# Performance work log

Hardware: AMD Instinct MI355X
Metric: run time of the kernel (lower is better)

Reference implementation:

```python
import jax, jax.numpy as jnp
import numpy as np

B, T, F, H = 512, 365, 16, 256


def _lstm_layer(x, W_ih, W_hh, b_ih, b_hh):
    """batch_first LSTM layer, torch gate order (i, f, g, o).
    x: [B, T, in]. Returns (outputs [B, T, H], final h [B, H])."""
    # Precompute input projections for all timesteps: [T, B, 4H]
    x_proj = jnp.einsum('bti,gi->tbg', x, W_ih) + (b_ih + b_hh)
    h0 = jnp.zeros((x.shape[0], W_hh.shape[1]), x.dtype)
    c0 = jnp.zeros_like(h0)

    def step(carry, xp):
        h, c = carry
        z = xp + h @ W_hh.T  # [B, 4H]
        i, f, g, o = jnp.split(z, 4, axis=-1)
        c = jax.nn.sigmoid(f) * c + jax.nn.sigmoid(i) * jnp.tanh(g)
        h = jax.nn.sigmoid(o) * jnp.tanh(c)
        return (h, c), h

    (hT, _), hs = jax.lax.scan(step, (h0, c0), x_proj)
    return jnp.transpose(hs, (1, 0, 2)), hT


def setup_inputs() -> dict:
    key = jax.random.key(0)
    ks = jax.random.split(key, 11)
    s1 = 1.0 / np.sqrt(H)
    u = lambda k, shape: jax.random.uniform(k, shape, jnp.float32, -s1, s1)
    return {
        'x': jax.random.normal(ks[0], (B, T, F), jnp.float32),
        'W_ih1': u(ks[1], (4 * H, F)),
        'W_hh1': u(ks[2], (4 * H, H)),
        'b_ih1': u(ks[3], (4 * H,)),
        'b_hh1': u(ks[4], (4 * H,)),
        'W_ih2': u(ks[5], (4 * H, H)),
        'W_hh2': u(ks[6], (4 * H, H)),
        'b_ih2': u(ks[7], (4 * H,)),
        'b_hh2': u(ks[8], (4 * H,)),
        'W_lin': u(ks[9], (1, H)),
        'b_lin': u(ks[10], (1,)),
    }


def reference(x, W_ih1, W_hh1, b_ih1, b_hh1, W_ih2, W_hh2, b_ih2, b_hh2, W_lin, b_lin):
    h1_seq, _ = _lstm_layer(x, W_ih1, W_hh1, b_ih1, b_hh1)
    # dropout(p=0.1) is identity in eval mode
    _, hT = _lstm_layer(h1_seq, W_ih2, W_hh2, b_ih2, b_hh2)
    out = (hT @ W_lin.T + b_lin).reshape(-1)  # [B]
    return out
```

## Files before the change

### kernel.cpp

```cpp
#include <hip/hip_runtime.h>


#define T_STEPS 365
#define RS 564

typedef __attribute__((ext_vector_type(8))) short short8;
typedef __attribute__((ext_vector_type(4))) float float4_;
typedef __attribute__((ext_vector_type(4))) unsigned int uint4_;
typedef unsigned long long u64;
typedef unsigned int u32;

#define MFMA16(a, b, c) __builtin_amdgcn_mfma_f32_16x16x32_bf16((a), (b), (c), 0, 0, 0)

__device__ __forceinline__ unsigned short f2bf(float v) {
    union { float f; u32 u; } a; a.f = v;
    u32 r = a.u + 0x7fffu + ((a.u >> 16) & 1u);
    return (unsigned short)(r >> 16);
}
__device__ __forceinline__ float bf2f(unsigned short h) {
    union { u32 u; float f; } a; a.u = ((u32)h) << 16; return a.f;
}
__device__ __forceinline__ u32 packhl(float v) {
    unsigned short hi = f2bf(v);
    unsigned short lo = f2bf(v - bf2f(hi));
    return ((u32)hi << 16) | (u32)lo;
}
__device__ __forceinline__ float sigm(float x)  { return 1.f / (1.f + __expf(-x)); }
__device__ __forceinline__ float tanh_(float x) { return 2.f / (1.f + __expf(-2.f * x)) - 1.f; }

__device__ __forceinline__ void unpk(uint4_ a, uint4_ b, short8& hi, short8& lo) {
    union U { u32 d[4]; short8 s; } H, L;
    H.d[0] = __builtin_amdgcn_perm(a.y, a.x, 0x07060302u);
    H.d[1] = __builtin_amdgcn_perm(a.w, a.z, 0x07060302u);
    H.d[2] = __builtin_amdgcn_perm(b.y, b.x, 0x07060302u);
    H.d[3] = __builtin_amdgcn_perm(b.w, b.z, 0x07060302u);
    L.d[0] = __builtin_amdgcn_perm(a.y, a.x, 0x05040100u);
    L.d[1] = __builtin_amdgcn_perm(a.w, a.z, 0x05040100u);
    L.d[2] = __builtin_amdgcn_perm(b.y, b.x, 0x05040100u);
    L.d[3] = __builtin_amdgcn_perm(b.w, b.z, 0x05040100u);
    hi = H.s; lo = L.s;
}

__global__ void prep_w(
    const float* __restrict__ Wih1, const float* __restrict__ Whh1,
    const float* __restrict__ bih1, const float* __restrict__ bhh1,
    const float* __restrict__ Wih2, const float* __restrict__ Whh2,
    const float* __restrict__ bih2, const float* __restrict__ bhh2,
    unsigned short* __restrict__ w1h, unsigned short* __restrict__ w1l,
    unsigned short* __restrict__ w2h, unsigned short* __restrict__ w2l,
    float* __restrict__ bias1, float* __restrict__ bias2)
{
    const int tile = blockIdx.x;
    const int g = tile >> 4, ns = tile & 15;
    const int tid = threadIdx.x;

    for (int idx = tid; idx < 9 * 512; idx += 256) {
        int ks = idx >> 9, off = idx & 511, r = off >> 5, kk = off & 31;
        int R = g * 256 + ns * 16 + r;
        float v;
        if (ks < 8)       v = Whh1[R * 256 + ks * 32 + kk];
        else if (kk < 16) v = Wih1[R * 16 + kk];
        else              v = 0.f;
        unsigned short h = f2bf(v);
        size_t d = (size_t)(tile * 9 + ks) * 512 + off;
        w1h[d] = h; w1l[d] = f2bf(v - bf2f(h));
    }
    for (int idx = tid; idx < 16 * 512; idx += 256) {
        int ks = idx >> 9, off = idx & 511, r = off >> 5, kk = off & 31;
        int R = g * 256 + ns * 16 + r;
        int k = ks * 32 + kk;
        float v = (k < 256) ? Wih2[R * 256 + k] : Whh2[R * 256 + (k - 256)];
        unsigned short h = f2bf(v);
        size_t d = (size_t)(tile * 16 + ks) * 512 + off;
        w2h[d] = h; w2l[d] = f2bf(v - bf2f(h));
    }
    if (tid < 16) {
        int R = g * 256 + ns * 16 + tid;
        bias1[R] = bih1[R] + bhh1[R];
        bias2[R] = bih2[R] + bhh2[R];
    }
}

__global__ __launch_bounds__(512, 2) void lstm_main(
    const float* __restrict__ x,
    const unsigned short* __restrict__ w1h, const unsigned short* __restrict__ w1l,
    const unsigned short* __restrict__ w2h, const unsigned short* __restrict__ w2l,
    const float* __restrict__ bias1, const float* __restrict__ bias2,
    u32* hb1, u32* hb2, u32* prog,
    const float* __restrict__ Wlin, const float* __restrict__ blin,
    float* __restrict__ out)
{
    __shared__ __align__(16) u32 A2u[32 * RS];
    __shared__ __align__(16) float zb1[3 * 64 * 36];
    __shared__ __align__(16) float zb2[5 * 64 * 36];
    __shared__ __align__(16) float hp[32][17];

    const int tid  = threadIdx.x;
    const int lane = tid & 63;
    const int wv   = tid >> 6;
    const int quad = lane >> 4;
    const int r16  = lane & 15;
    const int bg   = blockIdx.x & 15;
    const int ns   = blockIdx.x >> 4;

    u32* myprog = prog + bg * 16;

    const bool isL1 = (wv < 3);
    int t0, t1_, t2_, t3_;
    if      (wv == 0) { t0 = 0;  t1_ = 1;  t2_ = 2;  t3_ = -1; }
    else if (wv == 1) { t0 = 3;  t1_ = 4;  t2_ = 5;  t3_ = -1; }
    else if (wv == 2) { t0 = 6;  t1_ = 7;  t2_ = 8;  t3_ = -1; }
    else if (wv == 3) { t0 = 0;  t1_ = 1;  t2_ = 2;  t3_ = 3;  }
    else if (wv == 4) { t0 = 4;  t1_ = 5;  t2_ = 6;  t3_ = -1; }
    else if (wv == 5) { t0 = 7;  t1_ = 9;  t2_ = 10; t3_ = -1; }
    else if (wv == 6) { t0 = 11; t1_ = 12; t2_ = 13; t3_ = -1; }
    else              { t0 = 14; t1_ = 15; t2_ = 16; t3_ = -1; }

    const int loff = r16 * 32 + quad * 8;
    const unsigned short* WHsrc = isL1 ? w1h : w2h;
    const unsigned short* WLsrc = isL1 ? w1l : w2l;
    const int NK = isL1 ? 9 : 16;
    short8 WH[4][4], WL[4][4];
#pragma unroll
    for (int s = 0; s < 4; s++) {
        const int b = (s == 0) ? t0 : (s == 1) ? t1_ : (s == 2) ? t2_ : t3_;
#pragma unroll
        for (int g = 0; g < 4; g++) {
            if (b >= 0) {
                int ks = (!isL1 && b > 8) ? (b - 1) : b;
                size_t off = ((size_t)((g * 16 + ns) * NK + ks)) * 512 + loff;
                WH[g][s] = *(const short8*)(WHsrc + off);
                WL[g][s] = *(const short8*)(WLsrc + off);
            } else {
                WH[g][s] = short8{0,0,0,0,0,0,0,0};
                WL[g][s] = short8{0,0,0,0,0,0,0,0};
            }
        }
    }

    float bi[4] = {0.f, 0.f, 0.f, 0.f};
    if (tid < 256) {
        const float* bsrc = (tid < 128) ? bias1 : bias2;
        int colg = ns * 16 + (tid & 15);
#pragma unroll
        for (int g = 0; g < 4; g++) bi[g] = bsrc[g * 256 + colg];
    }
    float cst[4] = {0.f, 0.f, 0.f, 0.f};

    for (int i = tid; i < 32 * RS; i += 512) A2u[i] = 0u;
    __syncthreads();
    {
        int row = tid >> 4, col = tid & 15;
        float v = x[((size_t)(bg * 32 + row) * T_STEPS + 0) * 16 + col];
        A2u[row * RS + 256 + col] = packhl(v);
    }
    __syncthreads();

    for (int t = 0; t <= T_STEPS; t++) {
        const int p = t & 1;

        float4_ acc[4][2];
        const float4_ z4 = {0.f, 0.f, 0.f, 0.f};
#pragma unroll
        for (int g = 0; g < 4; g++) { acc[g][0] = z4; acc[g][1] = z4; }

#pragma unroll
        for (int s = 0; s < 4; s++) {
            const int b = (s == 0) ? t0 : (s == 1) ? t1_ : (s == 2) ? t2_ : t3_;
            if (b >= 0) {
                const int base0 = r16 * RS + b * 32 + quad * 8;
                uint4_ p00 = *(const uint4_*)&A2u[base0];
                uint4_ p01 = *(const uint4_*)&A2u[base0 + 4];
                uint4_ p10 = *(const uint4_*)&A2u[base0 + 16 * RS];
                uint4_ p11 = *(const uint4_*)&A2u[base0 + 16 * RS + 4];
                short8 ah0, al0, ah1, al1;
                unpk(p00, p01, ah0, al0);
                unpk(p10, p11, ah1, al1);
#pragma unroll
                for (int g = 0; g < 4; g++) {
                    acc[g][0] = MFMA16(ah0, WH[g][s], acc[g][0]);
                    acc[g][0] = MFMA16(al0, WH[g][s], acc[g][0]);
                    acc[g][0] = MFMA16(ah0, WL[g][s], acc[g][0]);
                    acc[g][1] = MFMA16(ah1, WH[g][s], acc[g][1]);
                    acc[g][1] = MFMA16(al1, WH[g][s], acc[g][1]);
                    acc[g][1] = MFMA16(ah1, WL[g][s], acc[g][1]);
                }
            }
        }
        {
            float* zbase = isL1 ? (zb1 + wv * (64 * 36)) : (zb2 + (wv - 3) * (64 * 36));
#pragma unroll
            for (int g = 0; g < 4; g++)
#pragma unroll
                for (int rt = 0; rt < 2; rt++)
                    *(float4_*)&zbase[(size_t)(g * 16 + r16) * 36 + rt * 16 + quad * 4] = acc[g][rt];
        }
        __syncthreads();

        if (tid < 256) {
            const bool is1 = (tid < 128);
            const int hcol = tid & 15;
            const int rq   = (tid >> 4) & 7;
            const float* zb = is1 ? zb1 : zb2;
            const int np = is1 ? 3 : 5;
            float4_ z[4];
#pragma unroll
            for (int g = 0; g < 4; g++) {
                float4_ s = {bi[g], bi[g], bi[g], bi[g]};
#pragma unroll
                for (int pw = 0; pw < 5; pw++) {
                    if (pw < np)
                        s += *(const float4_*)&zb[(size_t)(pw * 64 + g * 16 + hcol) * 36 + rq * 4];
                }
                z[g] = s;
            }
            u32* hb = is1 ? hb1 : hb2;
            const int slot = is1 ? p : (1 - p);
            size_t o = (((size_t)slot * 16 + bg) * 32 + rq * 4) * 256 + ns * 16 + hcol;
#pragma unroll
            for (int j = 0; j < 4; j++) {
                float zi = z[0][j], zf = z[1][j], zg = z[2][j], zo = z[3][j];
                float nc = sigm(zf) * cst[j] + sigm(zi) * tanh_(zg);
                float h  = sigm(zo) * tanh_(nc);
                if (!is1 && t == 0) { nc = 0.f; h = 0.f; }
                cst[j] = nc;
                __hip_atomic_store(&hb[o + (size_t)j * 256], packhl(h),
                                   __ATOMIC_RELAXED, __HIP_MEMORY_SCOPE_AGENT);
            }
        } else {
            const int i0 = tid - 256;
            const int tn = (t + 1 <= T_STEPS - 1) ? (t + 1) : (T_STEPS - 1);
#pragma unroll
            for (int k = 0; k < 2; k++) {
                int idx = i0 + 256 * k;
                int row = idx >> 4, col = idx & 15;
                float v = x[((size_t)(bg * 32 + row) * T_STEPS + tn) * 16 + col];
                A2u[row * RS + 256 + col] = packhl(v);
            }
        }
        __syncthreads();

        if (tid == 0)
            __hip_atomic_store(&myprog[ns], (u32)(t + 1),
                               __ATOMIC_RELAXED, __HIP_MEMORY_SCOPE_AGENT);

        if (t == T_STEPS) break;

        {
            const u32 tgt = (u32)(t + 1);
            while (__hip_atomic_load(&myprog[tid & 15], __ATOMIC_RELAXED,
                                     __HIP_MEMORY_SCOPE_AGENT) < tgt) {}
        }

        {
            const u64* s1 = (const u64*)(hb1 + (size_t)(p * 16 + bg) * 32 * 256);
            const u64* s2 = (const u64*)(hb2 + (size_t)((1 - p) * 16 + bg) * 32 * 256);
#pragma unroll
            for (int j = 0; j < 4; j++) {
                const int row = wv * 4 + j;
                const u64* r1 = s1 + (size_t)row * 128;
                const u64* r2 = s2 + (size_t)row * 128;
                u64 a = __hip_atomic_load(r1 + lane,      __ATOMIC_RELAXED, __HIP_MEMORY_SCOPE_AGENT);
                u64 b = __hip_atomic_load(r1 + 64 + lane, __ATOMIC_RELAXED, __HIP_MEMORY_SCOPE_AGENT);
                u64 c = __hip_atomic_load(r2 + lane,      __ATOMIC_RELAXED, __HIP_MEMORY_SCOPE_AGENT);
                u64 d = __hip_atomic_load(r2 + 64 + lane, __ATOMIC_RELAXED, __HIP_MEMORY_SCOPE_AGENT);
                u32* dst = &A2u[row * RS];
                *(u64*)&dst[2 * lane]             = a;
                *(u64*)&dst[128 + 2 * lane]       = b;
                *(u64*)&dst[288 + 2 * lane]       = c;
                *(u64*)&dst[288 + 128 + 2 * lane] = d;
            }
        }
        __syncthreads();
    }

    if (ns != 0) return;
    {
        const u32 tgt = (u32)(T_STEPS + 1);
        while (__hip_atomic_load(&myprog[tid & 15], __ATOMIC_RELAXED,
                                 __HIP_MEMORY_SCOPE_AGENT) < tgt) {}
    }
    {
        int row = tid >> 4, seg = tid & 15;
        const u32* src = hb2 + ((size_t)bg * 32 + row) * 256 + seg * 16;
        float s = 0.f;
#pragma unroll
        for (int j = 0; j < 16; j++) {
            u32 v = __hip_atomic_load(&src[j], __ATOMIC_RELAXED, __HIP_MEMORY_SCOPE_AGENT);
            s += (bf2f((unsigned short)(v >> 16)) + bf2f((unsigned short)v)) * Wlin[seg * 16 + j];
        }
        hp[row][seg] = s;
    }
    __syncthreads();
    if (tid < 32) {
        float s = 0.f;
#pragma unroll
        for (int j = 0; j < 16; j++) s += hp[tid][j];
        out[bg * 32 + tid] = s + blin[0];
    }
}

extern "C" void kernel_launch(void* const* d_in, const int* in_sizes, int n_in,
                              void* d_out, int out_size, void* d_ws, size_t ws_size,
                              hipStream_t stream) {
    const float* x    = (const float*)d_in[0];
    const float* Wih1 = (const float*)d_in[1];
    const float* Whh1 = (const float*)d_in[2];
    const float* bih1 = (const float*)d_in[3];
    const float* bhh1 = (const float*)d_in[4];
    const float* Wih2 = (const float*)d_in[5];
    const float* Whh2 = (const float*)d_in[6];
    const float* bih2 = (const float*)d_in[7];
    const float* bhh2 = (const float*)d_in[8];
    const float* Wlin = (const float*)d_in[9];
    const float* blin = (const float*)d_in[10];
    float* out = (float*)d_out;

    char* pp = (char*)d_ws;
    unsigned short* w1h = (unsigned short*)pp; pp += (size_t)64 * 9 * 512 * 2;
    unsigned short* w1l = (unsigned short*)pp; pp += (size_t)64 * 9 * 512 * 2;
    unsigned short* w2h = (unsigned short*)pp; pp += (size_t)64 * 16 * 512 * 2;
    unsigned short* w2l = (unsigned short*)pp; pp += (size_t)64 * 16 * 512 * 2;
    float* bias1 = (float*)pp; pp += 1024 * 4;
    float* bias2 = (float*)pp; pp += 1024 * 4;
    char* zero_base = pp;
    u32* hb1 = (u32*)pp; pp += (size_t)2 * 16 * 32 * 256 * 4;
    u32* hb2 = (u32*)pp; pp += (size_t)2 * 16 * 32 * 256 * 4;
    u32* prog = (u32*)pp; pp += 16 * 16 * 4;
    size_t zero_bytes = (size_t)(pp - zero_base);

    hipMemsetAsync(zero_base, 0, zero_bytes, stream);
    prep_w<<<64, 256, 0, stream>>>(Wih1, Whh1, bih1, bhh1, Wih2, Whh2, bih2, bhh2,
                                   w1h, w1l, w2h, w2l, bias1, bias2);
    lstm_main<<<256, 512, 0, stream>>>(x, w1h, w1l, w2h, w2l, bias1, bias2,
                                       hb1, hb2, prog, Wlin, blin, out);
}
```

Before: 2.003 ms.

## Split each batch group into two 16-row chains to overlap exchange with compute

Each block's 32 batch rows become two independent 16-row chains, with separate LDS buffers, progress flags and hidden-state slots. Chain B's GEMM and update run while chain A's cross-block hidden-state exchange is still propagating. Progress is now signalled per wave instead of after a block barrier. A single wave polls the flags with s_sleep and publishes readiness through LDS, so the other waves do not spin on global memory. The cost is more barriers and flag traffic per step, and the hidden-state and flag stores now use workgroup scope, which may weaken cross-block visibility.

```diff
diff --git a/kernel.cpp b/kernel.cpp
--- a/kernel.cpp
+++ b/kernel.cpp
@@ -11,6 +11,7 @@
 typedef unsigned int u32;
 
 #define MFMA16(a, b, c) __builtin_amdgcn_mfma_f32_16x16x32_bf16((a), (b), (c), 0, 0, 0)
+#define LD64(p) __hip_atomic_load((p), __ATOMIC_RELAXED, __HIP_MEMORY_SCOPE_AGENT)
 
 __device__ __forceinline__ unsigned short f2bf(float v) {
     union { float f; u32 u; } a; a.f = v;
@@ -90,10 +91,10 @@
     const float* __restrict__ Wlin, const float* __restrict__ blin,
     float* __restrict__ out)
 {
-    __shared__ __align__(16) u32 A2u[32 * RS];
-    __shared__ __align__(16) float zb1[3 * 64 * 36];
-    __shared__ __align__(16) float zb2[5 * 64 * 36];
+    __shared__ __align__(16) u32 Abuf[2][16 * RS];
+    __shared__ __align__(16) float zbuf[2][8 * 64 * 20];
     __shared__ __align__(16) float hp[32][17];
+    __shared__ u32 rdyv[2];
 
     const int tid  = threadIdx.x;
     const int lane = tid & 63;
@@ -102,8 +103,10 @@
     const int r16  = lane & 15;
     const int bg   = blockIdx.x & 15;
     const int ns   = blockIdx.x >> 4;
-
-    u32* myprog = prog + bg * 16;
+    const int ch0  = bg * 2;
+
+    u32* progA = prog + (size_t)ch0 * 256;
+    u32* progB = prog + (size_t)(ch0 + 1) * 256;
 
     const bool isL1 = (wv < 3);
     int t0, t1_, t2_, t3_;
@@ -138,151 +141,172 @@
         }
     }
 
-    float bi[4] = {0.f, 0.f, 0.f, 0.f};
+    const bool is1u = (tid < 256);
+    const int hcol = tid & 15;
+    const int urow = (tid >> 4) & 15;
+    float bi[4];
+    {
+        const float* bsrc = is1u ? bias1 : bias2;
+        int colg = ns * 16 + hcol;
+#pragma unroll
+        for (int g = 0; g < 4; g++) bi[g] = bsrc[g * 256 + colg];
+    }
+    float cstA = 0.f, cstB = 0.f;
+
+    for (int i = tid; i < 2 * 16 * RS; i += 512) (&Abuf[0][0])[i] = 0u;
+    if (tid < 2) rdyv[tid] = 0u;
+    __syncthreads();
     if (tid < 256) {
-        const float* bsrc = (tid < 128) ? bias1 : bias2;
-        int colg = ns * 16 + (tid & 15);
-#pragma unroll
-        for (int g = 0; g < 4; g++) bi[g] = bsrc[g * 256 + colg];
-    }
-    float cst[4] = {0.f, 0.f, 0.f, 0.f};
-
-    for (int i = tid; i < 32 * RS; i += 512) A2u[i] = 0u;
+        int row = tid >> 4, col = tid & 15;
+        float va = x[((size_t)(bg * 32 + row) * T_STEPS + 0) * 16 + col];
+        float vb = x[((size_t)(bg * 32 + 16 + row) * T_STEPS + 0) * 16 + col];
+        Abuf[0][row * RS + 256 + col] = packhl(va);
+        Abuf[1][row * RS + 256 + col] = packhl(vb);
+    }
     __syncthreads();
-    {
-        int row = tid >> 4, col = tid & 15;
-        float v = x[((size_t)(bg * 32 + row) * T_STEPS + 0) * 16 + col];
-        A2u[row * RS + 256 + col] = packhl(v);
-    }
-    __syncthreads();
+
+#define GEMM_AND_STORE(cidx) do {                                             \
+        float4_ acc[4];                                                       \
+        const float4_ z4 = {0.f, 0.f, 0.f, 0.f};                              \
+        acc[0] = z4; acc[1] = z4; acc[2] = z4; acc[3] = z4;                   \
+        __builtin_amdgcn_s_setprio(1);                                        \
+        _Pragma("unroll")                                                     \
+        for (int s = 0; s < 4; s++) {                                         \
+            const int b = (s == 0) ? t0 : (s == 1) ? t1_ : (s == 2) ? t2_ : t3_; \
+            if (b >= 0) {                                                     \
+                const int base0 = r16 * RS + b * 32 + quad * 8;               \
+                uint4_ p00 = *(const uint4_*)&Abuf[cidx][base0];              \
+                uint4_ p01 = *(const uint4_*)&Abuf[cidx][base0 + 4];          \
+                short8 ah0, al0;                                              \
+                unpk(p00, p01, ah0, al0);                                     \
+                _Pragma("unroll")                                             \
+                for (int g = 0; g < 4; g++) {                                 \
+                    acc[g] = MFMA16(ah0, WH[g][s], acc[g]);                   \
+                    acc[g] = MFMA16(al0, WH[g][s], acc[g]);                   \
+                    acc[g] = MFMA16(ah0, WL[g][s], acc[g]);                   \
+                }                                                             \
+            }                                                                 \
+        }                                                                     \
+        __builtin_amdgcn_s_setprio(0);                                        \
+        _Pragma("unroll")                                                     \
+        for (int g = 0; g < 4; g++)                                           \
+            *(float4_*)&zbuf[cidx][wv * 1280 + (g * 16 + r16) * 20 + quad * 4] = acc[g]; \
+    } while (0)
+
+#define UPDATE_CHAIN(cidx, cstVar, progPtr, ch) do {                          \
+        const float* zb = &zbuf[cidx][(is1u ? 0 : 3) * 1280];                 \
+        const int np = is1u ? 3 : 5;                                          \
+        float z[4];                                                           \
+        _Pragma("unroll")                                                     \
+        for (int g = 0; g < 4; g++) {                                         \
+            float s = bi[g];                                                  \
+            _Pragma("unroll")                                                 \
+            for (int pw = 0; pw < 5; pw++)                                    \
+                if (pw < np)                                                  \
+                    s += zb[pw * 1280 + (g * 16 + hcol) * 20 + urow];         \
+            z[g] = s;                                                         \
+        }                                                                     \
+        u32* hb = is1u ? hb1 : hb2;                                           \
+        const int slot = is1u ? p : (1 - p);                                  \
+        size_t o = (((size_t)slot * 32 + (ch)) * 16 + urow) * 256 + ns * 16 + hcol; \
+        float nc = sigm(z[1]) * cstVar + sigm(z[0]) * tanh_(z[2]);            \
+        float h  = sigm(z[3]) * tanh_(nc);                                    \
+        if (!is1u && t == 0) { nc = 0.f; h = 0.f; }                           \
+        cstVar = nc;                                                          \
+        __hip_atomic_store(&hb[o], packhl(h),                                 \
+                           __ATOMIC_RELAXED, __HIP_MEMORY_SCOPE_WORKGROUP);   \
+        asm volatile("s_waitcnt vmcnt(0)" ::: "memory");                      \
+        if (lane == 0)                                                        \
+            __hip_atomic_store(&(progPtr)[ns * 16 + wv], (u32)(t + 1),        \
+                               __ATOMIC_RELAXED, __HIP_MEMORY_SCOPE_WORKGROUP); \
+    } while (0)
+
+#define POLL_CHAIN(progPtr, ri) do {                                          \
+        const u32 tgt = (u32)(t + 1);                                         \
+        if (wv == 7) {                                                        \
+            const int f1 = (lane >> 2) * 16 + (lane & 3);                     \
+            const int f2 = f1 + 4;                                            \
+            for (;;) {                                                        \
+                u32 a = __hip_atomic_load(&(progPtr)[f1], __ATOMIC_RELAXED,   \
+                                          __HIP_MEMORY_SCOPE_AGENT);          \
+                u32 b = __hip_atomic_load(&(progPtr)[f2], __ATOMIC_RELAXED,   \
+                                          __HIP_MEMORY_SCOPE_AGENT);          \
+                if (a >= tgt && b >= tgt) break;                              \
+                __builtin_amdgcn_s_sleep(1);                                  \
+            }                                                                 \
+            if (lane == 0)                                                    \
+                __hip_atomic_store(&rdyv[ri], tgt, __ATOMIC_RELEASE,          \
+                                   __HIP_MEMORY_SCOPE_WORKGROUP);             \
+        } else {                                                              \
+            while (__hip_atomic_load(&rdyv[ri], __ATOMIC_ACQUIRE,             \
+                                     __HIP_MEMORY_SCOPE_WORKGROUP) < tgt) {}  \
+        }                                                                     \
+    } while (0)
+
+#define RESTAGE_CHAIN(cidx, ch) do {                                          \
+        const u64* s1 = (const u64*)hb1 + ((size_t)(p * 32 + (ch))) * 2048;   \
+        const u64* s2 = (const u64*)hb2 + ((size_t)((1 - p) * 32 + (ch))) * 2048; \
+        _Pragma("unroll")                                                     \
+        for (int j = 0; j < 2; j++) {                                         \
+            const int row = wv * 2 + j;                                       \
+            const u64* r1 = s1 + (size_t)row * 128;                           \
+            const u64* r2 = s2 + (size_t)row * 128;                           \
+            u64 a = LD64(r1 + lane);                                          \
+            u64 b = LD64(r1 + 64 + lane);                                     \
+            u64 c = LD64(r2 + lane);                                          \
+            u64 d = LD64(r2 + 64 + lane);                                     \
+            u32* dst = &Abuf[cidx][row * RS];                                 \
+            *(u64*)&dst[2 * lane]             = a;                            \
+            *(u64*)&dst[128 + 2 * lane]       = b;                            \
+            *(u64*)&dst[288 + 2 * lane]       = c;                            \
+            *(u64*)&dst[288 + 128 + 2 * lane] = d;                            \
+        }                                                                     \
+        if (tid < 256) {                                                      \
+            int row = tid >> 4, col = tid & 15;                               \
+            const int tn = (t + 1 <= T_STEPS - 1) ? (t + 1) : (T_STEPS - 1);  \
+            float v = x[((size_t)(bg * 32 + (cidx) * 16 + row) * T_STEPS + tn) * 16 + col]; \
+            Abuf[cidx][row * RS + 256 + col] = packhl(v);                     \
+        }                                                                     \
+    } while (0)
 
     for (int t = 0; t <= T_STEPS; t++) {
         const int p = t & 1;
 
-        float4_ acc[4][2];
-        const float4_ z4 = {0.f, 0.f, 0.f, 0.f};
-#pragma unroll
-        for (int g = 0; g < 4; g++) { acc[g][0] = z4; acc[g][1] = z4; }
-
-#pragma unroll
-        for (int s = 0; s < 4; s++) {
-            const int b = (s == 0) ? t0 : (s == 1) ? t1_ : (s == 2) ? t2_ : t3_;
-            if (b >= 0) {
-                const int base0 = r16 * RS + b * 32 + quad * 8;
-                uint4_ p00 = *(const uint4_*)&A2u[base0];
-                uint4_ p01 = *(const uint4_*)&A2u[base0 + 4];
-                uint4_ p10 = *(const uint4_*)&A2u[base0 + 16 * RS];
-                uint4_ p11 = *(const uint4_*)&A2u[base0 + 16 * RS + 4];
-                short8 ah0, al0, ah1, al1;
-                unpk(p00, p01, ah0, al0);
-                unpk(p10, p11, ah1, al1);
-#pragma unroll
-                for (int g = 0; g < 4; g++) {
-                    acc[g][0] = MFMA16(ah0, WH[g][s], acc[g][0]);
-                    acc[g][0] = MFMA16(al0, WH[g][s], acc[g][0]);
-                    acc[g][0] = MFMA16(ah0, WL[g][s], acc[g][0]);
-                    acc[g][1] = MFMA16(ah1, WH[g][s], acc[g][1]);
-                    acc[g][1] = MFMA16(al1, WH[g][s], acc[g][1]);
-                    acc[g][1] = MFMA16(ah1, WL[g][s], acc[g][1]);
-                }
-            }
-        }
-        {
-            float* zbase = isL1 ? (zb1 + wv * (64 * 36)) : (zb2 + (wv - 3) * (64 * 36));
-#pragma unroll
-            for (int g = 0; g < 4; g++)
-#pragma unroll
-                for (int rt = 0; rt < 2; rt++)
-                    *(float4_*)&zbase[(size_t)(g * 16 + r16) * 36 + rt * 16 + quad * 4] = acc[g][rt];
-        }
+        GEMM_AND_STORE(0);
         __syncthreads();
-
-        if (tid < 256) {
-            const bool is1 = (tid < 128);
-            const int hcol = tid & 15;
-            const int rq   = (tid >> 4) & 7;
-            const float* zb = is1 ? zb1 : zb2;
-            const int np = is1 ? 3 : 5;
-            float4_ z[4];
-#pragma unroll
-            for (int g = 0; g < 4; g++) {
-                float4_ s = {bi[g], bi[g], bi[g], bi[g]};
-#pragma unroll
-                for (int pw = 0; pw < 5; pw++) {
-                    if (pw < np)
-                        s += *(const float4_*)&zb[(size_t)(pw * 64 + g * 16 + hcol) * 36 + rq * 4];
-                }
-                z[g] = s;
-            }
-            u32* hb = is1 ? hb1 : hb2;
-            const int slot = is1 ? p : (1 - p);
-            size_t o = (((size_t)slot * 16 + bg) * 32 + rq * 4) * 256 + ns * 16 + hcol;
-#pragma unroll
-            for (int j = 0; j < 4; j++) {
-                float zi = z[0][j], zf = z[1][j], zg = z[2][j], zo = z[3][j];
-                float nc = sigm(zf) * cst[j] + sigm(zi) * tanh_(zg);
-                float h  = sigm(zo) * tanh_(nc);
-                if (!is1 && t == 0) { nc = 0.f; h = 0.f; }
-                cst[j] = nc;
-                __hip_atomic_store(&hb[o + (size_t)j * 256], packhl(h),
-                                   __ATOMIC_RELAXED, __HIP_MEMORY_SCOPE_AGENT);
-            }
-        } else {
-            const int i0 = tid - 256;
-            const int tn = (t + 1 <= T_STEPS - 1) ? (t + 1) : (T_STEPS - 1);
-#pragma unroll
-            for (int k = 0; k < 2; k++) {
-                int idx = i0 + 256 * k;
-                int row = idx >> 4, col = idx & 15;
-                float v = x[((size_t)(bg * 32 + row) * T_STEPS + tn) * 16 + col];
-                A2u[row * RS + 256 + col] = packhl(v);
-            }
-        }
+        UPDATE_CHAIN(0, cstA, progA, ch0);
+
+        GEMM_AND_STORE(1);
         __syncthreads();
-
-        if (tid == 0)
-            __hip_atomic_store(&myprog[ns], (u32)(t + 1),
-                               __ATOMIC_RELAXED, __HIP_MEMORY_SCOPE_AGENT);
+        UPDATE_CHAIN(1, cstB, progB, ch0 + 1);
 
         if (t == T_STEPS) break;
 
-        {
-            const u32 tgt = (u32)(t + 1);
-            while (__hip_atomic_load(&myprog[tid & 15], __ATOMIC_RELAXED,
-                                     __HIP_MEMORY_SCOPE_AGENT) < tgt) {}
-        }
-
-        {
-            const u64* s1 = (const u64*)(hb1 + (size_t)(p * 16 + bg) * 32 * 256);
-            const u64* s2 = (const u64*)(hb2 + (size_t)((1 - p) * 16 + bg) * 32 * 256);
-#pragma unroll
-            for (int j = 0; j < 4; j++) {
-                const int row = wv * 4 + j;
-                const u64* r1 = s1 + (size_t)row * 128;
-                const u64* r2 = s2 + (size_t)row * 128;
-                u64 a = __hip_atomic_load(r1 + lane,      __ATOMIC_RELAXED, __HIP_MEMORY_SCOPE_AGENT);
-                u64 b = __hip_atomic_load(r1 + 64 + lane, __ATOMIC_RELAXED, __HIP_MEMORY_SCOPE_AGENT);
-                u64 c = __hip_atomic_load(r2 + lane,      __ATOMIC_RELAXED, __HIP_MEMORY_SCOPE_AGENT);
-                u64 d = __hip_atomic_load(r2 + 64 + lane, __ATOMIC_RELAXED, __HIP_MEMORY_SCOPE_AGENT);
-                u32* dst = &A2u[row * RS];
-                *(u64*)&dst[2 * lane]             = a;
-                *(u64*)&dst[128 + 2 * lane]       = b;
-                *(u64*)&dst[288 + 2 * lane]       = c;
-                *(u64*)&dst[288 + 128 + 2 * lane] = d;
-            }
-        }
+        POLL_CHAIN(progA, 0);
+        RESTAGE_CHAIN(0, ch0);
+        POLL_CHAIN(progB, 1);
+        RESTAGE_CHAIN(1, ch0 + 1);
         __syncthreads();
     }
 
     if (ns != 0) return;
     {
         const u32 tgt = (u32)(T_STEPS + 1);
-        while (__hip_atomic_load(&myprog[tid & 15], __ATOMIC_RELAXED,
-                                 __HIP_MEMORY_SCOPE_AGENT) < tgt) {}
+        const int f1 = (lane >> 2) * 16 + (lane & 3);
+        const int f2 = f1 + 4;
+        for (;;) {
+            u32 a = __hip_atomic_load(&progA[f1], __ATOMIC_RELAXED, __HIP_MEMORY_SCOPE_AGENT);
+            u32 b = __hip_atomic_load(&progA[f2], __ATOMIC_RELAXED, __HIP_MEMORY_SCOPE_AGENT);
+            u32 c = __hip_atomic_load(&progB[f1], __ATOMIC_RELAXED, __HIP_MEMORY_SCOPE_AGENT);
+            u32 d = __hip_atomic_load(&progB[f2], __ATOMIC_RELAXED, __HIP_MEMORY_SCOPE_AGENT);
+            if (a >= tgt && b >= tgt && c >= tgt && d >= tgt) break;
+            __builtin_amdgcn_s_sleep(1);
+        }
     }
     {
         int row = tid >> 4, seg = tid & 15;
-        const u32* src = hb2 + ((size_t)bg * 32 + row) * 256 + seg * 16;
+        int ch = ch0 + (row >> 4), r = row & 15;
+        const u32* src = hb2 + ((size_t)(0 * 32 + ch) * 16 + r) * 256 + seg * 16;
         float s = 0.f;
 #pragma unroll
         for (int j = 0; j < 16; j++) {
@@ -324,9 +348,9 @@
     float* bias1 = (float*)pp; pp += 1024 * 4;
     float* bias2 = (float*)pp; pp += 1024 * 4;
     char* zero_base = pp;
-    u32* hb1 = (u32*)pp; pp += (size_t)2 * 16 * 32 * 256 * 4;
-    u32* hb2 = (u32*)pp; pp += (size_t)2 * 16 * 32 * 256 * 4;
-    u32* prog = (u32*)pp; pp += 16 * 16 * 4;
+    u32* hb1 = (u32*)pp; pp += (size_t)2 * 32 * 16 * 256 * 4;
+    u32* hb2 = (u32*)pp; pp += (size_t)2 * 32 * 16 * 256 * 4;
+    u32* prog = (u32*)pp; pp += (size_t)32 * 256 * 4;
     size_t zero_bytes = (size_t)(pp - zero_base);
 
     hipMemsetAsync(zero_base, 0, zero_bytes, stream);
```

After: 1.796 ms. -10.4%, faster.
